# Kernel tuning notes

Measured on AMD Instinct MI355X. Metric: run time of the kernel, lower is better.

## Reference

```python
import jax, jax.numpy as jnp
import numpy as np
from jax import lax

H = 384
W = 384
N = H * W                 # flattened pixel count
N_LOC = N // 2            # unknown pixels with 3x3 matting-Laplacian stencils
KCM = 20                  # color-mixture KNN size
K_IU = 5                  # intra-unknown KNN size
NNZ_CM = N_LOC * KCM


def setup_inputs() -> dict:
    key = jax.random.key(0)
    ks = jax.random.split(key, 16)
    f32 = jnp.float32
    i32 = jnp.int32
    inp = {}
    inp["CM_weights"] = jax.random.uniform(ks[0], (N,), f32)
    inp["LOC_weights"] = jax.random.uniform(ks[1], (N,), f32)
    inp["IU_weights"] = jax.random.uniform(ks[2], (N,), f32)
    inp["KU_weights"] = jax.random.uniform(ks[3], (N,), f32)
    inp["lmbda"] = jnp.full((1,), 100.0, f32)
    inp["kToUconf"] = jax.random.uniform(ks[4], (N,), f32)
    inp["known"] = jax.random.uniform(ks[5], (N,), f32)
    inp["kToU"] = jax.random.uniform(ks[6], (N,), f32)
    inp["Wcm_data"] = jax.random.uniform(ks[7], (NNZ_CM,), f32)
    inp["LOC_flows"] = jax.random.uniform(ks[8], (9, 9, N_LOC), f32)
    inp["IU_flows"] = jax.random.uniform(ks[9], (N_LOC, K_IU), f32)
    inp["Wcm_row"] = jax.random.randint(ks[10], (NNZ_CM,), 0, N, dtype=i32)
    inp["Wcm_col"] = jax.random.randint(ks[11], (NNZ_CM,), 0, N, dtype=i32)
    # interior pixels so all 9 stencil neighbours are valid
    inp["LOC_inInd"] = jax.random.randint(ks[12], (N_LOC,), W + 1, N - W - 1, dtype=i32)
    inp["IU_inInd"] = jax.random.randint(ks[13], (N_LOC,), 0, N, dtype=i32)
    inp["IU_neighInd"] = jax.random.randint(ks[14], (N_LOC, K_IU), 0, N, dtype=i32)
    inp["width"] = W
    inp["cg_steps"] = 30
    return inp


def reference(CM_weights, LOC_weights, IU_weights, KU_weights, lmbda,
              kToUconf, known, kToU, Wcm_data, LOC_flows, IU_flows,
              Wcm_row, Wcm_col, LOC_inInd, IU_inInd, IU_neighInd,
              width, cg_steps):
    n = kToU.shape[0]
    seg = lambda v, i: jax.ops.segment_sum(v, i, num_segments=n)

    # --- color mixture: Wcm scaled by diag(CM_weights); L = diag(rowsum) - Wcm; Lcm = L^T L
    cm_vals = CM_weights[Wcm_row] * Wcm_data
    rs_cm = seg(cm_vals, Wcm_row)

    # --- matting Laplacian: 9x9 flows per unknown pixel over 3x3 stencil
    offs = jnp.array([-1 - width, -1, -1 + width, -width, 0, width,
                      1 - width, 1, 1 + width], dtype=LOC_inInd.dtype)
    neigh = LOC_inInd[:, None] + offs[None, :]                    # [n_loc, 9]
    fl = LOC_flows * LOC_weights[LOC_inInd][None, None, :]        # [9, 9, n_loc]
    nloc = neigh.shape[0]
    # entry (row=neigh[k,i], col=neigh[k,j]) has value fl[j, i, k]
    vals_m = jnp.transpose(fl, (2, 1, 0)).reshape(-1)
    rows_m = jnp.broadcast_to(neigh[:, :, None], (nloc, 9, 9)).reshape(-1)
    cols_m = jnp.broadcast_to(neigh[:, None, :], (nloc, 9, 9)).reshape(-1)
    rows_ms = jnp.concatenate([rows_m, cols_m])
    cols_ms = jnp.concatenate([cols_m, rows_m])
    vals_ms = 0.5 * jnp.concatenate([vals_m, vals_m])             # W = 0.5 (W + W^T)
    rs_m = seg(vals_ms, rows_ms)

    # --- intra-unknowns KNN affinities
    fiu = IU_flows * IU_weights[IU_inInd][:, None]                # [n_iu, K]
    rows_c0 = jnp.broadcast_to(IU_inInd[:, None], IU_neighInd.shape).reshape(-1)
    cols_c0 = IU_neighInd.reshape(-1)
    rows_cs = jnp.concatenate([rows_c0, cols_c0])
    cols_cs = jnp.concatenate([cols_c0, rows_c0])
    vals_cs = 0.5 * jnp.concatenate([fiu.reshape(-1), fiu.reshape(-1)])
    rs_c = seg(vals_cs, rows_cs)

    # --- diagonal data terms: KU + lmbda*known
    diag_ku = KU_weights * kToUconf + lmbda[0] * known
    b = diag_ku * kToU

    def matvec(v):
        # Lcm @ v = L^T (L v), keeping L in factored COO form
        Lv = rs_cm * v - seg(cm_vals * v[Wcm_col], Wcm_row)
        lcm = rs_cm * Lv - seg(cm_vals * Lv[Wcm_row], Wcm_col)
        lm = rs_m * v - seg(vals_ms * v[cols_ms], rows_ms)
        lc = rs_c * v - seg(vals_cs * v[cols_cs], rows_cs)
        return lcm + lm + lc + diag_ku * v

    def cg_step(carry, _):
        x, r, p, rs = carry
        Ap = matvec(p)
        alpha = rs / jnp.vdot(p, Ap)
        x = x + alpha * p
        r = r - alpha * Ap
        rs_new = jnp.vdot(r, r)
        p = r + (rs_new / rs) * p
        return (x, r, p, rs_new), None

    x0 = jnp.zeros_like(b)  # x0 = 0 as in MattingSolver
    (x, _, _, _), _ = lax.scan(cg_step, (x0, b, b, jnp.vdot(b, b)), None, length=cg_steps)
    return x
```

## Files before the change

### kernel.cpp

```cpp
#include <hip/hip_runtime.h>


#define TPB 256

__device__ __forceinline__ float blockReduce256(float v) {
  #pragma unroll
  for (int o = 32; o > 0; o >>= 1) v += __shfl_down(v, o, 64);
  __shared__ float s[4];
  int lane = threadIdx.x & 63, wv = threadIdx.x >> 6;
  if (lane == 0) s[wv] = v;
  __syncthreads();
  return (threadIdx.x == 0) ? (s[0] + s[1] + s[2] + s[3]) : 0.f;
}

__global__ void k_init0(const float* __restrict__ KUw, const float* __restrict__ kToUconf,
                        const float* __restrict__ lmbda, const float* __restrict__ known,
                        const float* __restrict__ kToU,
                        float* __restrict__ diag_ku, float2* __restrict__ PR,
                        float* __restrict__ x,
                        int* __restrict__ CNT, float* __restrict__ scal, int N)
{
  int i = blockIdx.x * TPB + threadIdx.x;
  if (i < 80) scal[i] = 0.f;
  if (i < 4 * N) CNT[i] = 0;
  float red = 0.f;
  if (i < N) {
    float dk = KUw[i] * kToUconf[i] + lmbda[0] * known[i];
    diag_ku[i] = dk;
    float b = dk * kToU[i];
    PR[i] = make_float2(b, b);
    x[i] = 0.f;
    red = b * b;
  }
  float v = blockReduce256(red);
  if (threadIdx.x == 0) atomicAdd(&scal[0], v);
}

__global__ void k_prep(float* __restrict__ LOC_flows, const int* __restrict__ LOC_inInd,
                       const float* __restrict__ LOCw, int NLOC)
{
  int k = blockIdx.x * TPB + threadIdx.x;
  float Fl[81];
  #pragma unroll
  for (int m = 0; m < 81; ++m) Fl[m] = LOC_flows[(size_t)m * NLOC + k];
  float hw = 0.5f * LOCw[LOC_inInd[k]];
  int idx = 0;
  #pragma unroll
  for (int a = 0; a < 9; ++a)
    #pragma unroll
    for (int b = a + 1; b < 9; ++b) {
      LOC_flows[(size_t)idx * NLOC + k] = hw * (Fl[a * 9 + b] + Fl[b * 9 + a]);
      ++idx;
    }
}

__global__ void k_sh(const int* __restrict__ LOC_inInd, int* __restrict__ CNT,
                     unsigned short* __restrict__ sTick, int N, int NLOC)
{
  int k = blockIdx.x * TPB + threadIdx.x;
  sTick[k] = (unsigned short)atomicAdd(&CNT[3 * N + LOC_inInd[k]], 1);
}

__global__ void k_wminit(int* __restrict__ CNT, const int* __restrict__ width_p, int N)
{
  int j = blockIdx.x * TPB + threadIdx.x;
  int wd = *width_p;
  const int offs[9] = {-1 - wd, -1, -1 + wd, -wd, 0, wd, 1 - wd, 1, 1 + wd};
  int s = 0;
  #pragma unroll
  for (int a = 0; a < 9; ++a) {
    int v = j - offs[a];
    if (v >= 0 && v < N) s += CNT[3 * N + v];
  }
  CNT[2 * N + j] = s;
}

__global__ void k_hist(const int* __restrict__ Wrow, const int* __restrict__ Wcol,
                       const int* __restrict__ IU_inInd, const int* __restrict__ IU_neighInd,
                       int* __restrict__ CNT,
                       unsigned short* __restrict__ tr, unsigned short* __restrict__ tc,
                       unsigned short* __restrict__ tU,
                       int NLOC, int N, int B0)
{
  int blk = blockIdx.x;
  if (blk < B0) {
    int e = blk * TPB + threadIdx.x;
    tr[e] = (unsigned short)atomicAdd(&CNT[Wrow[e]], 1);
    tc[e] = (unsigned short)atomicAdd(&CNT[N + Wcol[e]], 1);
  } else {
    int k = (blk - B0) * TPB + threadIdx.x;
    tU[5 * NLOC + k] = (unsigned short)atomicAdd(&CNT[2 * N + IU_inInd[k]], 1);
    #pragma unroll
    for (int j = 0; j < 5; ++j)
      tU[j * NLOC + k] =
          (unsigned short)atomicAdd(&CNT[2 * N + IU_neighInd[k * 5 + j]], 1);
  }
}

__global__ void k_scan1(int* __restrict__ OFF, int* __restrict__ bsum, int tot)
{
  __shared__ int s[TPB];
  int gid = blockIdx.x * TPB + threadIdx.x;
  int v = (gid < tot) ? OFF[gid] : 0;
  s[threadIdx.x] = v;
  __syncthreads();
  #pragma unroll
  for (int o = 1; o < TPB; o <<= 1) {
    int t = (threadIdx.x >= o) ? s[threadIdx.x - o] : 0;
    __syncthreads();
    s[threadIdx.x] += t;
    __syncthreads();
  }
  if (gid < tot) OFF[gid] = s[threadIdx.x] - v;
  if (threadIdx.x == TPB - 1) bsum[blockIdx.x] = s[threadIdx.x];
}

__global__ void k_scan2(int* __restrict__ bsum, int nPerArr)
{
  __shared__ int s[1024];
  int base = blockIdx.x * nPerArr;
  int v = (threadIdx.x < nPerArr) ? bsum[base + threadIdx.x] : 0;
  s[threadIdx.x] = v;
  __syncthreads();
  for (int o = 1; o < 1024; o <<= 1) {
    int t = (threadIdx.x >= o) ? s[threadIdx.x - o] : 0;
    __syncthreads();
    s[threadIdx.x] += t;
    __syncthreads();
  }
  if (threadIdx.x < nPerArr) bsum[base + threadIdx.x] = s[threadIdx.x] - v;
}

__global__ void k_scan3(int* __restrict__ OFF, const int* __restrict__ bsum, int tot)
{
  int gid = blockIdx.x * TPB + threadIdx.x;
  if (gid < tot) OFF[gid] += bsum[blockIdx.x];
}

__global__ void k_sc(const int* __restrict__ LOC_inInd, const int* __restrict__ OFF,
                     const unsigned short* __restrict__ sTick,
                     int* __restrict__ perm, int* __restrict__ LOC_inIndP,
                     int N, int NLOC)
{
  int k = blockIdx.x * TPB + threadIdx.x;
  int v = LOC_inInd[k];
  int pos = OFF[3 * N + v] + sTick[k];
  perm[pos] = k;
  LOC_inIndP[pos] = v;
}

__global__ void k_permS2(float* __restrict__ LOC_flows, const int* __restrict__ perm,
                         int NLOC)
{
  int kp = blockIdx.x * TPB + threadIdx.x;
  int k = perm[kp];
  #pragma unroll
  for (int m = 0; m < 36; ++m)
    LOC_flows[(size_t)(36 + m) * NLOC + kp] = LOC_flows[(size_t)m * NLOC + k];
}

__global__ void k_fill(const float* __restrict__ CMw, const float* __restrict__ Wcm_data,
                       const int* __restrict__ Wrow, const int* __restrict__ Wcol,
                       const int* __restrict__ LOC_inIndP, const int* __restrict__ width_p,
                       const int* __restrict__ IU_inInd, const int* __restrict__ IU_neighInd,
                       const int* __restrict__ OFF,
                       const unsigned short* __restrict__ tr, const unsigned short* __restrict__ tc,
                       const unsigned short* __restrict__ tU,
                       int2* __restrict__ csrPk, int2* __restrict__ cscPk,
                       int* __restrict__ gU,
                       int NLOC, int N, int B0, int B1)
{
  int blk = blockIdx.x;
  if (blk < B0) {
    int e = blk * TPB + threadIdx.x;
    int row = Wrow[e], col = Wcol[e];
    int cv = __float_as_int(CMw[row] * Wcm_data[e]);
    csrPk[OFF[row] + tr[e]] = make_int2(col, cv);
    cscPk[OFF[N + col] + tc[e]] = make_int2(row, cv);
  } else if (blk < B1) {
    int kp = (blk - B0) * TPB + threadIdx.x;
    int wd = *width_p;
    int base = LOC_inIndP[kp];
    const int* cum = OFF + 3 * N;
    int rank = kp - cum[base];
    int hh[5][5];
    #pragma unroll
    for (int dr = 0; dr < 5; ++dr) {
      int c[6];
      #pragma unroll
      for (int m = 0; m < 6; ++m) {
        int v = base + (dr - 2) * wd + (m - 2);
        c[m] = (v <= 0) ? 0 : ((v >= N) ? NLOC : cum[v]);
      }
      #pragma unroll
      for (int m = 0; m < 5; ++m) hh[dr][m] = c[m + 1] - c[m];
    }
    const int CAv[9] = {-1, -1, -1, 0, 0, 0, 1, 1, 1};
    const int RAv[9] = {-1, 0, 1, -1, 0, 1, -1, 0, 1};
    #pragma unroll
    for (int a = 0; a < 9; ++a) {
      int T = 0;
      #pragma unroll
      for (int ap = 0; ap < a; ++ap)
        T += hh[RAv[a] - RAv[ap] + 2][CAv[a] - CAv[ap] + 2];
      int j = base + CAv[a] + RAv[a] * wd;
      gU[OFF[2 * N + j] + T + rank] = a * NLOC + kp;
    }
  } else {
    int k = (blk - B1) * TPB + threadIdx.x;
    gU[OFF[2 * N + IU_inInd[k]] + tU[5 * NLOC + k]] = 14 * NLOC + k;
    #pragma unroll
    for (int j = 0; j < 5; ++j)
      gU[OFF[2 * N + IU_neighInd[k * 5 + j]] + tU[j * NLOC + k]] =
          (9 + j) * NLOC + k;
  }
}

__global__ void k_it1(const float2* __restrict__ PR,
                      const float* __restrict__ S2p, const int* __restrict__ LOC_inIndP,
                      const int* __restrict__ width_p,
                      const float* __restrict__ IU_flows, const int* __restrict__ IU_inInd,
                      const int* __restrict__ IU_neighInd, const float* __restrict__ IUw,
                      const float* __restrict__ diag_ku,
                      const int* __restrict__ OFF, const int2* __restrict__ csrPk,
                      float* __restrict__ u_all,
                      float* __restrict__ Lv, float* __restrict__ rs_cm,
                      const float* __restrict__ rsN, const float* __restrict__ rsO, int first,
                      float* __restrict__ pAp_t,
                      int NNZ, int NLOC, int N, int B0, int B1)
{
  int blk = blockIdx.x;
  float beta = first ? 0.f : rsN[0] / rsO[0];
  float red = 0.f;
  if (blk < B0) {
    int kp = blk * TPB + threadIdx.x;
    int wd = *width_p;
    int base = LOC_inIndP[kp];
    const int offs[9] = {-1 - wd, -1, -1 + wd, -wd, 0, wd, 1 - wd, 1, 1 + wd};
    float pv[9];
    #pragma unroll
    for (int a = 0; a < 9; ++a) {
      float2 pr = PR[base + offs[a]];
      pv[a] = __builtin_fmaf(beta, pr.x, pr.y);
    }
    float u[9] = {0.f, 0.f, 0.f, 0.f, 0.f, 0.f, 0.f, 0.f, 0.f};
    float qf = 0.f;
    int idx = 0;
    #pragma unroll
    for (int a = 0; a < 9; ++a)
      #pragma unroll
      for (int b = a + 1; b < 9; ++b) {
        float sv = S2p[(size_t)idx * NLOC + kp];
        ++idx;
        float d = pv[a] - pv[b];
        float t = sv * d;
        u[a] += t; u[b] -= t;
        qf += t * d;
      }
    #pragma unroll
    for (int a = 0; a < 9; ++a) u_all[a * NLOC + kp] = u[a];
    red = qf;
  } else if (blk < B1) {
    int k = (blk - B0) * TPB + threadIdx.x;
    int r0 = IU_inInd[k];
    float hw = 0.5f * IUw[r0];
    float2 prr = PR[r0];
    float pr = __builtin_fmaf(beta, prr.x, prr.y);
    int c[5]; float w[5];
    #pragma unroll
    for (int j = 0; j < 5; ++j) {
      c[j] = IU_neighInd[k * 5 + j];
      w[j] = hw * IU_flows[k * 5 + j];
    }
    float pc[5];
    #pragma unroll
    for (int j = 0; j < 5; ++j) {
      float2 pp = PR[c[j]];
      pc[j] = __builtin_fmaf(beta, pp.x, pp.y);
    }
    float qf = 0.f, asum = 0.f;
    #pragma unroll
    for (int j = 0; j < 5; ++j) {
      float d = pr - pc[j];
      float uA = w[j] * d;
      u_all[(9 + j) * NLOC + k] = -uA;
      asum += uA;
      qf += uA * d;
    }
    u_all[14 * NLOC + k] = asum;
    red = qf;
  } else {
    int i = (blk - B1) * TPB + threadIdx.x;
    float2 pri = PR[i];
    float pi = __builtin_fmaf(beta, pri.x, pri.y);
    int s = OFF[i];
    int e = (i == N - 1) ? NNZ : OFF[i + 1];
    float acc = 0.f, rs = 0.f;
    int q = s;
    for (; q + 8 <= e; q += 8) {
      int2 ed[8];
      #pragma unroll
      for (int m = 0; m < 8; ++m) ed[m] = csrPk[q + m];
      float g[8];
      #pragma unroll
      for (int m = 0; m < 8; ++m) {
        float2 pp = PR[ed[m].x];
        g[m] = __builtin_fmaf(beta, pp.x, pp.y);
      }
      #pragma unroll
      for (int m = 0; m < 8; ++m) {
        float cv = __int_as_float(ed[m].y);
        rs += cv;
        acc += cv * (pi - g[m]);
      }
    }
    for (; q + 4 <= e; q += 4) {
      int2 ed[4];
      #pragma unroll
      for (int m = 0; m < 4; ++m) ed[m] = csrPk[q + m];
      float g[4];
      #pragma unroll
      for (int m = 0; m < 4; ++m) {
        float2 pp = PR[ed[m].x];
        g[m] = __builtin_fmaf(beta, pp.x, pp.y);
      }
      #pragma unroll
      for (int m = 0; m < 4; ++m) {
        float cv = __int_as_float(ed[m].y);
        rs += cv;
        acc += cv * (pi - g[m]);
      }
    }
    for (; q < e; ++q) {
      int2 ed = csrPk[q];
      float cv = __int_as_float(ed.y);
      float2 pp = PR[ed.x];
      rs += cv;
      acc += cv * (pi - __builtin_fmaf(beta, pp.x, pp.y));
    }
    Lv[i] = acc;
    rs_cm[i] = rs;
    red = diag_ku[i] * pi * pi + acc * acc;
  }
  float v = blockReduce256(red);
  if (threadIdx.x == 0) atomicAdd(pAp_t, v);
}

__global__ void k_it2(float* __restrict__ x, float2* __restrict__ PR,
                      const float* __restrict__ Lv,
                      const float* __restrict__ rs_cm, const float* __restrict__ diag_ku,
                      const int* __restrict__ OFF,
                      const int2* __restrict__ cscPk,
                      const int* __restrict__ gU, const float* __restrict__ u_all,
                      const float* __restrict__ rs_t, const float* __restrict__ pAp_t,
                      const float* __restrict__ rsO, int first,
                      float* __restrict__ rs_t1,
                      int NNZ, int NLOC, int N)
{
  int i = blockIdx.x * TPB + threadIdx.x;
  float alpha = rs_t[0] / pAp_t[0];
  float beta = first ? 0.f : rs_t[0] / rsO[0];
  float tg = 0.f;
  {
    int s0 = OFF[2 * N + i];
    int e0 = (i == N - 1) ? 15 * NLOC : OFF[2 * N + i + 1];
    int q = s0;
    for (; q + 8 <= e0; q += 8) {
      int g[8];
      #pragma unroll
      for (int m = 0; m < 8; ++m) g[m] = gU[q + m];
      float u[8];
      #pragma unroll
      for (int m = 0; m < 8; ++m) u[m] = u_all[g[m]];
      #pragma unroll
      for (int m = 0; m < 8; ++m) tg += u[m];
    }
    for (; q + 4 <= e0; q += 4) {
      int g[4];
      #pragma unroll
      for (int m = 0; m < 4; ++m) g[m] = gU[q + m];
      float u[4];
      #pragma unroll
      for (int m = 0; m < 4; ++m) u[m] = u_all[g[m]];
      #pragma unroll
      for (int m = 0; m < 4; ++m) tg += u[m];
    }
    for (; q < e0; ++q) tg += u_all[gU[q]];
  }
  float sc = 0.f;
  {
    int s0 = OFF[N + i];
    int e0 = (i == N - 1) ? NNZ : OFF[N + i + 1];
    int q = s0;
    for (; q + 8 <= e0; q += 8) {
      int2 ed[8];
      #pragma unroll
      for (int m = 0; m < 8; ++m) ed[m] = cscPk[q + m];
      float l[8];
      #pragma unroll
      for (int m = 0; m < 8; ++m) l[m] = Lv[ed[m].x];
      #pragma unroll
      for (int m = 0; m < 8; ++m) sc += __int_as_float(ed[m].y) * l[m];
    }
    for (; q + 4 <= e0; q += 4) {
      int2 ed[4];
      #pragma unroll
      for (int m = 0; m < 4; ++m) ed[m] = cscPk[q + m];
      float l[4];
      #pragma unroll
      for (int m = 0; m < 4; ++m) l[m] = Lv[ed[m].x];
      #pragma unroll
      for (int m = 0; m < 4; ++m) sc += __int_as_float(ed[m].y) * l[m];
    }
    for (; q < e0; ++q) {
      int2 ed = cscPk[q];
      sc += __int_as_float(ed.y) * Lv[ed.x];
    }
  }
  float2 pri = PR[i];
  float pi = __builtin_fmaf(beta, pri.x, pri.y);
  float Ap = diag_ku[i] * pi + rs_cm[i] * Lv[i] - sc + tg;
  x[i] += alpha * pi;
  float rn = pri.y - alpha * Ap;
  PR[i] = make_float2(pi, rn);
  float v = blockReduce256(rn * rn);
  if (threadIdx.x == 0) atomicAdd(rs_t1, v);
}

extern "C" void kernel_launch(void* const* d_in, const int* in_sizes, int n_in,
                              void* d_out, int out_size, void* d_ws, size_t ws_size,
                              hipStream_t stream)
{
  const float* CMw       = (const float*)d_in[0];
  const float* LOCw      = (const float*)d_in[1];
  const float* IUw       = (const float*)d_in[2];
  const float* KUw       = (const float*)d_in[3];
  const float* lmbda     = (const float*)d_in[4];
  const float* kToUconf  = (const float*)d_in[5];
  const float* known     = (const float*)d_in[6];
  const float* kToU      = (const float*)d_in[7];
  const float* Wcm_data  = (const float*)d_in[8];
  float*       LOC_flows = (float*)d_in[9];
  const float* IU_flows  = (const float*)d_in[10];
  const int*   Wrow      = (const int*)d_in[11];
  const int*   Wcol      = (const int*)d_in[12];
  const int*   LOC_inInd = (const int*)d_in[13];
  const int*   IU_inInd  = (const int*)d_in[14];
  const int*   IU_neighInd = (const int*)d_in[15];
  const int*   width_p   = (const int*)d_in[16];
  const int CG_STEPS = 30;

  const int N    = in_sizes[0];
  const int NNZ  = in_sizes[8];
  const int NLOC = in_sizes[13];

  float* x       = (float*)d_out;
  float2* PR     = (float2*)d_ws;
  float* Lv      = (float*)(PR + (size_t)N);
  float* rs_cm   = Lv + N;
  float* diag_ku = rs_cm + N;
  int2*  csrPk   = (int2*)(diag_ku + N);
  int2*  cscPk   = csrPk + (size_t)NNZ;
  int*   gU      = (int*)(cscPk + (size_t)NNZ);
  int*   OFF     = gU + (size_t)15 * NLOC;
  unsigned short* tr = (unsigned short*)(OFF + (size_t)4 * N);
  unsigned short* tc = tr + (size_t)NNZ;
  unsigned short* tU = tc + (size_t)NNZ;
  float* u_all   = (float*)tr;
  int*   bsum    = (int*)(tU + (size_t)6 * NLOC);
  float* scal    = (float*)(bsum + 4 * (N / TPB));
  int*   perm    = (int*)(scal + 80);
  int*   LOC_inIndP = perm + NLOC;
  unsigned short* sTick = (unsigned short*)(LOC_inIndP + NLOC);

  const int Bn = N / TPB;
  const int Bz = NNZ / TPB;
  const int Bl = NLOC / TPB;
  const int Z4 = 4 * Bn;

  k_init0<<<Z4, TPB, 0, stream>>>(KUw, kToUconf, lmbda, known, kToU,
                                  diag_ku, PR, x, OFF, scal, N);
  k_prep<<<Bl, TPB, 0, stream>>>(LOC_flows, LOC_inInd, LOCw, NLOC);
  k_sh<<<Bl, TPB, 0, stream>>>(LOC_inInd, OFF, sTick, N, NLOC);
  k_wminit<<<Bn, TPB, 0, stream>>>(OFF, width_p, N);
  k_hist<<<Bz + Bl, TPB, 0, stream>>>(Wrow, Wcol, IU_inInd, IU_neighInd, OFF,
                                      tr, tc, tU, NLOC, N, Bz);
  k_scan1<<<Z4, TPB, 0, stream>>>(OFF, bsum, 4 * N);
  k_scan2<<<4, 1024, 0, stream>>>(bsum, Bn);
  k_scan3<<<Z4, TPB, 0, stream>>>(OFF, bsum, 4 * N);
  k_sc<<<Bl, TPB, 0, stream>>>(LOC_inInd, OFF, sTick, perm, LOC_inIndP, N, NLOC);
  k_permS2<<<Bl, TPB, 0, stream>>>(LOC_flows, perm, NLOC);
  k_fill<<<Bz + 2 * Bl, TPB, 0, stream>>>(CMw, Wcm_data, Wrow, Wcol,
                                          LOC_inIndP, width_p, IU_inInd, IU_neighInd,
                                          OFF, tr, tc, tU,
                                          csrPk, cscPk, gU,
                                          NLOC, N, Bz, Bz + Bl);

  const float* S2p = LOC_flows + (size_t)36 * NLOC;
  for (int t = 0; t < CG_STEPS; ++t) {
    const float* rsN = scal + t;
    const float* rsO = scal + (t == 0 ? 0 : t - 1);
    k_it1<<<2 * Bl + Bn, TPB, 0, stream>>>(
        PR, S2p, LOC_inIndP, width_p,
        IU_flows, IU_inInd, IU_neighInd, IUw,
        diag_ku, OFF, csrPk, u_all, Lv, rs_cm,
        rsN, rsO, (t == 0) ? 1 : 0, scal + 40 + t,
        NNZ, NLOC, N, Bl, 2 * Bl);
    k_it2<<<Bn, TPB, 0, stream>>>(
        x, PR, Lv, rs_cm, diag_ku, OFF, cscPk, gU, u_all,
        rsN, scal + 40 + t, rsO, (t == 0) ? 1 : 0, scal + t + 1,
        NNZ, NLOC, N);
  }
}
```

Baseline: 1.753 ms.

## Build CSR/CSC for color-mixture matrix via two-level bucketed counting sort

Replaces the global-atomic histogram and scatter used to build the CSR and CSC copies of the color-mixture matrix with a two-pass bucketed counting sort. Each block first builds per-block histograms over coarse 256-row buckets in shared memory, scans them globally, and scatters entries to bucket segments. A final per-bucket kernel then sorts entries by row inside shared memory and writes the row offsets. This aims to cut contended global atomics and random writes in setup, at the cost of more launches, extra passes over the data, and an assumption that each bucket holds at most 4096 entries.

```diff
diff --git a/kernel.cpp b/kernel.cpp
--- a/kernel.cpp
+++ b/kernel.cpp
@@ -75,26 +75,16 @@
   CNT[2 * N + j] = s;
 }
 
-__global__ void k_hist(const int* __restrict__ Wrow, const int* __restrict__ Wcol,
-                       const int* __restrict__ IU_inInd, const int* __restrict__ IU_neighInd,
-                       int* __restrict__ CNT,
-                       unsigned short* __restrict__ tr, unsigned short* __restrict__ tc,
-                       unsigned short* __restrict__ tU,
-                       int NLOC, int N, int B0)
-{
-  int blk = blockIdx.x;
-  if (blk < B0) {
-    int e = blk * TPB + threadIdx.x;
-    tr[e] = (unsigned short)atomicAdd(&CNT[Wrow[e]], 1);
-    tc[e] = (unsigned short)atomicAdd(&CNT[N + Wcol[e]], 1);
-  } else {
-    int k = (blk - B0) * TPB + threadIdx.x;
-    tU[5 * NLOC + k] = (unsigned short)atomicAdd(&CNT[2 * N + IU_inInd[k]], 1);
-    #pragma unroll
-    for (int j = 0; j < 5; ++j)
-      tU[j * NLOC + k] =
-          (unsigned short)atomicAdd(&CNT[2 * N + IU_neighInd[k * 5 + j]], 1);
-  }
+__global__ void k_hist(const int* __restrict__ IU_inInd, const int* __restrict__ IU_neighInd,
+                       int* __restrict__ CNT, unsigned short* __restrict__ tU,
+                       int NLOC, int N)
+{
+  int k = blockIdx.x * TPB + threadIdx.x;
+  tU[5 * NLOC + k] = (unsigned short)atomicAdd(&CNT[2 * N + IU_inInd[k]], 1);
+  #pragma unroll
+  for (int j = 0; j < 5; ++j)
+    tU[j * NLOC + k] =
+        (unsigned short)atomicAdd(&CNT[2 * N + IU_neighInd[k * 5 + j]], 1);
 }
 
 __global__ void k_scan1(int* __restrict__ OFF, int* __restrict__ bsum, int tot)
@@ -159,26 +149,109 @@
     LOC_flows[(size_t)(36 + m) * NLOC + kp] = LOC_flows[(size_t)m * NLOC + k];
 }
 
-__global__ void k_fill(const float* __restrict__ CMw, const float* __restrict__ Wcm_data,
-                       const int* __restrict__ Wrow, const int* __restrict__ Wcol,
-                       const int* __restrict__ LOC_inIndP, const int* __restrict__ width_p,
+__global__ void kA_cnt(const int* __restrict__ Wrow, const int* __restrict__ Wcol,
+                       int* __restrict__ blockCnt, int NB1)
+{
+  __shared__ int h[1152];
+  for (int m = threadIdx.x; m < 1152; m += TPB) h[m] = 0;
+  __syncthreads();
+  int base = blockIdx.x * 4096;
+  #pragma unroll
+  for (int m = 0; m < 16; ++m) {
+    int e = base + m * TPB + threadIdx.x;
+    atomicAdd(&h[Wrow[e] >> 8], 1);
+    atomicAdd(&h[576 + (Wcol[e] >> 8)], 1);
+  }
+  __syncthreads();
+  for (int m = threadIdx.x; m < 1152; m += TPB)
+    blockCnt[m * NB1 + blockIdx.x] = h[m];
+}
+
+__global__ void kC_scatter(const float* __restrict__ CMw, const float* __restrict__ Wcm_data,
+                           const int* __restrict__ Wrow, const int* __restrict__ Wcol,
+                           const int* __restrict__ blockCnt,
+                           int2* __restrict__ csrPk, int2* __restrict__ cscPk,
+                           unsigned short* __restrict__ bRowR,
+                           unsigned short* __restrict__ bRowC,
+                           int NNZ, int NB1)
+{
+  __shared__ int cnt[1152];
+  for (int m = threadIdx.x; m < 1152; m += TPB) cnt[m] = 0;
+  __syncthreads();
+  int base = blockIdx.x * 4096;
+  #pragma unroll
+  for (int m = 0; m < 16; ++m) {
+    int e = base + m * TPB + threadIdx.x;
+    int row = Wrow[e], col = Wcol[e];
+    int cv = __float_as_int(CMw[row] * Wcm_data[e]);
+    int bR = row >> 8, bC = col >> 8;
+    int rR = atomicAdd(&cnt[bR], 1);
+    int rC = atomicAdd(&cnt[576 + bC], 1);
+    int sR = blockCnt[bR * NB1 + blockIdx.x] + rR;
+    int sC = blockCnt[(576 + bC) * NB1 + blockIdx.x] + rC - NNZ;
+    csrPk[sR] = make_int2(col, cv);
+    bRowR[sR] = (unsigned short)(row & 255);
+    cscPk[sC] = make_int2(row, cv);
+    bRowC[sC] = (unsigned short)(col & 255);
+  }
+}
+
+__global__ void kD_fin(const int* __restrict__ blockCnt,
+                       int2* __restrict__ csrPk, int2* __restrict__ cscPk,
+                       const unsigned short* __restrict__ bRowR,
+                       const unsigned short* __restrict__ bRowC,
+                       int* __restrict__ OFF, int NNZ, int N, int NB1)
+{
+  __shared__ unsigned short rw[4096];
+  __shared__ int2 en[4096];
+  __shared__ int hist[256];
+  __shared__ int sc[256];
+  int blk = blockIdx.x;
+  int side = blk / 576, b = blk % 576;
+  const unsigned short* bRow = side ? bRowC : bRowR;
+  int2* pk = side ? cscPk : csrPk;
+  int segBase = blockCnt[(side * 576 + b) * NB1] - side * NNZ;
+  int segEnd  = (b == 575) ? NNZ
+                           : (blockCnt[(side * 576 + b + 1) * NB1] - side * NNZ);
+  int len = segEnd - segBase;
+  for (int m = threadIdx.x; m < len; m += TPB) {
+    rw[m] = bRow[segBase + m];
+    en[m] = pk[segBase + m];
+  }
+  hist[threadIdx.x] = 0;
+  __syncthreads();
+  for (int m = threadIdx.x; m < len; m += TPB) atomicAdd(&hist[rw[m]], 1);
+  __syncthreads();
+  int v = hist[threadIdx.x];
+  sc[threadIdx.x] = v;
+  __syncthreads();
+  #pragma unroll
+  for (int o = 1; o < 256; o <<= 1) {
+    int t = (threadIdx.x >= o) ? sc[threadIdx.x - o] : 0;
+    __syncthreads();
+    sc[threadIdx.x] += t;
+    __syncthreads();
+  }
+  int cumv = sc[threadIdx.x] - v;
+  OFF[side * N + b * 256 + threadIdx.x] = segBase + cumv;
+  hist[threadIdx.x] = cumv;
+  __syncthreads();
+  for (int m = threadIdx.x; m < len; m += TPB) {
+    int pos = atomicAdd(&hist[rw[m]], 1);
+    pk[segBase + pos] = en[m];
+  }
+}
+
+__global__ void k_fill(const int* __restrict__ LOC_inIndP, const int* __restrict__ width_p,
                        const int* __restrict__ IU_inInd, const int* __restrict__ IU_neighInd,
                        const int* __restrict__ OFF,
-                       const unsigned short* __restrict__ tr, const unsigned short* __restrict__ tc,
                        const unsigned short* __restrict__ tU,
-                       int2* __restrict__ csrPk, int2* __restrict__ cscPk,
                        int* __restrict__ gU,
-                       int NLOC, int N, int B0, int B1)
+                       int NLOC, int N, int B0)
 {
   int blk = blockIdx.x;
   if (blk < B0) {
-    int e = blk * TPB + threadIdx.x;
-    int row = Wrow[e], col = Wcol[e];
-    int cv = __float_as_int(CMw[row] * Wcm_data[e]);
-    csrPk[OFF[row] + tr[e]] = make_int2(col, cv);
-    cscPk[OFF[N + col] + tc[e]] = make_int2(row, cv);
-  } else if (blk < B1) {
-    int kp = (blk - B0) * TPB + threadIdx.x;
+    int kp = blk * TPB + threadIdx.x;
     int wd = *width_p;
     int base = LOC_inIndP[kp];
     const int* cum = OFF + 3 * N;
@@ -207,7 +280,7 @@
       gU[OFF[2 * N + j] + T + rank] = a * NLOC + kp;
     }
   } else {
-    int k = (blk - B1) * TPB + threadIdx.x;
+    int k = (blk - B0) * TPB + threadIdx.x;
     gU[OFF[2 * N + IU_inInd[k]] + tU[5 * NLOC + k]] = 14 * NLOC + k;
     #pragma unroll
     for (int j = 0; j < 5; ++j)
@@ -472,29 +545,41 @@
   int*   perm    = (int*)(scal + 80);
   int*   LOC_inIndP = perm + NLOC;
   unsigned short* sTick = (unsigned short*)(LOC_inIndP + NLOC);
+  int*   blockCnt = (int*)(sTick + (size_t)NLOC);
 
   const int Bn = N / TPB;
-  const int Bz = NNZ / TPB;
   const int Bl = NLOC / TPB;
   const int Z4 = 4 * Bn;
+  const int NB1 = NNZ / 4096;
+  const int SC  = 1152 * NB1;
+  int* bsum1 = blockCnt + SC;
+  int* bsum2 = bsum1 + (SC + TPB - 1) / TPB;
+  const int SCB  = (SC + TPB - 1) / TPB;
+  const int SCB2 = (SCB + TPB - 1) / TPB;
 
   k_init0<<<Z4, TPB, 0, stream>>>(KUw, kToUconf, lmbda, known, kToU,
                                   diag_ku, PR, x, OFF, scal, N);
   k_prep<<<Bl, TPB, 0, stream>>>(LOC_flows, LOC_inInd, LOCw, NLOC);
   k_sh<<<Bl, TPB, 0, stream>>>(LOC_inInd, OFF, sTick, N, NLOC);
   k_wminit<<<Bn, TPB, 0, stream>>>(OFF, width_p, N);
-  k_hist<<<Bz + Bl, TPB, 0, stream>>>(Wrow, Wcol, IU_inInd, IU_neighInd, OFF,
-                                      tr, tc, tU, NLOC, N, Bz);
+  k_hist<<<Bl, TPB, 0, stream>>>(IU_inInd, IU_neighInd, OFF, tU, NLOC, N);
   k_scan1<<<Z4, TPB, 0, stream>>>(OFF, bsum, 4 * N);
   k_scan2<<<4, 1024, 0, stream>>>(bsum, Bn);
   k_scan3<<<Z4, TPB, 0, stream>>>(OFF, bsum, 4 * N);
   k_sc<<<Bl, TPB, 0, stream>>>(LOC_inInd, OFF, sTick, perm, LOC_inIndP, N, NLOC);
   k_permS2<<<Bl, TPB, 0, stream>>>(LOC_flows, perm, NLOC);
-  k_fill<<<Bz + 2 * Bl, TPB, 0, stream>>>(CMw, Wcm_data, Wrow, Wcol,
-                                          LOC_inIndP, width_p, IU_inInd, IU_neighInd,
-                                          OFF, tr, tc, tU,
-                                          csrPk, cscPk, gU,
-                                          NLOC, N, Bz, Bz + Bl);
+  kA_cnt<<<NB1, TPB, 0, stream>>>(Wrow, Wcol, blockCnt, NB1);
+  k_scan1<<<SCB, TPB, 0, stream>>>(blockCnt, bsum1, SC);
+  k_scan1<<<SCB2, TPB, 0, stream>>>(bsum1, bsum2, SCB);
+  k_scan2<<<1, 1024, 0, stream>>>(bsum2, SCB2);
+  k_scan3<<<SCB2, TPB, 0, stream>>>(bsum1, bsum2, SCB);
+  k_scan3<<<SCB, TPB, 0, stream>>>(blockCnt, bsum1, SC);
+  kC_scatter<<<NB1, TPB, 0, stream>>>(CMw, Wcm_data, Wrow, Wcol, blockCnt,
+                                      csrPk, cscPk, tr, tc, NNZ, NB1);
+  kD_fin<<<1152, TPB, 0, stream>>>(blockCnt, csrPk, cscPk, tr, tc,
+                                   OFF, NNZ, N, NB1);
+  k_fill<<<2 * Bl, TPB, 0, stream>>>(LOC_inIndP, width_p, IU_inInd, IU_neighInd,
+                                     OFF, tU, gU, NLOC, N, Bl);
 
   const float* S2p = LOC_flows + (size_t)36 * NLOC;
   for (int t = 0; t < CG_STEPS; ++t) {
```

New measurement: 1.755 ms. Within noise of the previous version (+0.1%).
